# Kernel tuning notes

Hardware: AMD Instinct MI355X
Metric: run time of the kernel (lower is better)

Reference implementation:

```python
import jax, jax.numpy as jnp
import numpy as np

N_NODES = 100000
N_EDGES = 3200000
N_GRAPHS = 512
DIM_H = 128
N_LAYERS = 3
N_CLASSES = 10
BN_EPS = 1e-5


def setup_inputs() -> dict:
    key = jax.random.key(0)
    ks = jax.random.split(key, 16)
    s = 1.0 / np.sqrt(DIM_H)
    x = jax.random.normal(ks[0], (N_NODES, DIM_H), dtype=jnp.float32)
    edge_index = jax.random.randint(ks[1], (2, N_EDGES), 0, N_NODES, dtype=jnp.int64)
    batch = jnp.sort(jax.random.randint(ks[2], (N_NODES,), 0, N_GRAPHS, dtype=jnp.int64))
    W1 = jax.random.uniform(ks[3], (N_LAYERS, DIM_H, DIM_H), jnp.float32, -s, s)
    b1 = jax.random.uniform(ks[4], (N_LAYERS, DIM_H), jnp.float32, -s, s)
    gamma = jnp.ones((N_LAYERS, DIM_H), jnp.float32)
    beta = jnp.zeros((N_LAYERS, DIM_H), jnp.float32)
    rmean = 0.1 * jax.random.normal(ks[5], (N_LAYERS, DIM_H), dtype=jnp.float32)
    rvar = jax.random.uniform(ks[6], (N_LAYERS, DIM_H), jnp.float32, 0.5, 1.5)
    W2 = jax.random.uniform(ks[7], (N_LAYERS, DIM_H, DIM_H), jnp.float32, -s, s)
    b2 = jax.random.uniform(ks[8], (N_LAYERS, DIM_H), jnp.float32, -s, s)
    dcat = DIM_H * N_LAYERS
    sf = 1.0 / np.sqrt(dcat)
    Wfin = jax.random.uniform(ks[9], (dcat, dcat), jnp.float32, -sf, sf)
    bfin = jax.random.uniform(ks[10], (dcat,), jnp.float32, -sf, sf)
    Wout = jax.random.uniform(ks[11], (dcat, N_CLASSES), jnp.float32, -sf, sf)
    bout = jax.random.uniform(ks[12], (N_CLASSES,), jnp.float32, -sf, sf)
    return {"x": x, "edge_index": edge_index, "batch": batch, "num_layers": N_LAYERS,
            "W1": W1, "b1": b1, "gamma": gamma, "beta": beta, "rmean": rmean, "rvar": rvar,
            "W2": W2, "b2": b2, "Wfin": Wfin, "bfin": bfin, "Wout": Wout, "bout": bout}


def reference(x, edge_index, batch, num_layers, W1, b1, gamma, beta, rmean, rvar, W2, b2, Wfin, bfin, Wout, bout):
    src, dst = edge_index[0], edge_index[1]
    h = x
    pooled = []
    for i in range(num_layers):
        # GINConv (eps=0): MLP(x + sum_{j in N(i)} x_j)
        aggr = jax.ops.segment_sum(h[src], dst, num_segments=N_NODES)
        z = (h + aggr) @ W1[i] + b1[i]
        # BatchNorm1d in eval mode (running stats)
        z = gamma[i] * (z - rmean[i]) * jax.lax.rsqrt(rvar[i] + BN_EPS) + beta[i]
        z = jax.nn.relu(z)
        h = jax.nn.relu(z @ W2[i] + b2[i])
        # global_add_pool: segment-sum over graph ids
        pooled.append(jax.ops.segment_sum(h, batch, num_segments=N_GRAPHS))
    h_fin = jnp.concatenate(pooled, axis=1)  # [G, dim_h*num_layers]
    h_fin = jax.nn.relu(h_fin @ Wfin + bfin)
    # dropout p=0.5 is identity in eval mode
    logits = h_fin @ Wout + bout
    return logits, jax.nn.log_softmax(logits, axis=1)
```

## Files before the change

kernel.cpp:

```cpp
#include <hip/hip_runtime.h>
#include <stdint.h>

#define N_NODES 100000
#define N_EDGES 3200000
#define N_GRAPHS 512
#define DIM 128
#define M_PAD 100096
#define NGB (M_PAD / 256)
#define NBUCK 391
#define CAP 9216
#define TILE 4096
#define NTILE 782
#define XMM_NB 392

typedef __bf16 bf16x8 __attribute__((ext_vector_type(8)));
typedef float f32x4 __attribute__((ext_vector_type(4)));

__device__ __forceinline__ unsigned short f2bf(float f) {
  unsigned u = __float_as_uint(f);
  u = u + 0x7FFFu + ((u >> 16) & 1u);
  return (unsigned short)(u >> 16);
}
__device__ __forceinline__ float bflo(unsigned v) { return __uint_as_float(v << 16); }
__device__ __forceinline__ float bfhi(unsigned v) { return __uint_as_float(v & 0xFFFF0000u); }
__device__ __forceinline__ unsigned packbf(float a, float b) {
  return (unsigned)f2bf(a) | ((unsigned)f2bf(b) << 16);
}

__global__ void k_zero32(int* __restrict__ p, int n) {
  int i = blockIdx.x * 256 + threadIdx.x;
  if (i < n) p[i] = 0;
}

__global__ __launch_bounds__(256) void k_bucket(const int* __restrict__ ei,
                                                int* __restrict__ cnt,
                                                unsigned* __restrict__ rec) {
  __shared__ int hist[NBUCK];
  __shared__ int curs[NBUCK];
  int t = threadIdx.x;
  int base_e = blockIdx.x * TILE;
  int es[16], ed[16];
#pragma unroll
  for (int k = 0; k < 16; ++k) {
    int e = base_e + k * 256 + t;
    if (e < N_EDGES) { es[k] = ei[e]; ed[k] = ei[N_EDGES + e]; }
    else ed[k] = -1;
  }
  for (int i = t; i < NBUCK; i += 256) hist[i] = 0;
  __syncthreads();
#pragma unroll
  for (int k = 0; k < 16; ++k)
    if (ed[k] >= 0) atomicAdd(&hist[ed[k] >> 8], 1);
  __syncthreads();
  for (int i = t; i < NBUCK; i += 256) {
    int h = hist[i];
    int g = h ? atomicAdd(&cnt[i], h) : 0;
    curs[i] = i * CAP + g;
  }
  __syncthreads();
#pragma unroll
  for (int k = 0; k < 16; ++k) {
    if (ed[k] >= 0) {
      int b = ed[k] >> 8;
      int pos = atomicAdd(&curs[b], 1);
      rec[pos] = ((unsigned)es[k] << 8) | (unsigned)(ed[k] & 255);
    }
  }
}

__global__ __launch_bounds__(512) void k_bscan(const int* __restrict__ cnt,
                                               int* __restrict__ bbase,
                                               int* __restrict__ row_ptr) {
  __shared__ int sc[512];
  int t = threadIdx.x;
  int tot = (t < NBUCK) ? min(cnt[t], CAP) : 0;
  sc[t] = tot; __syncthreads();
  for (int off = 1; off < 512; off <<= 1) {
    int x = (t >= off) ? sc[t - off] : 0;
    __syncthreads();
    sc[t] += x;
    __syncthreads();
  }
  if (t < NBUCK) bbase[t] = sc[t] - tot;
  if (t == NBUCK - 1) {
    bbase[NBUCK] = sc[t];
    row_ptr[N_NODES] = sc[t];
  }
}

__global__ __launch_bounds__(256) void k_build(const unsigned* __restrict__ rec,
                                               const int* __restrict__ cnt,
                                               const int* __restrict__ bbase,
                                               int* __restrict__ row_ptr,
                                               int* __restrict__ col) {
  __shared__ int hist[256];
  __shared__ int sc[256];
  __shared__ int curs[256];
  int b = blockIdx.x, t = threadIdx.x;
  int n = min(cnt[b], CAP);
  const unsigned* p = rec + (size_t)b * CAP;
  hist[t] = 0; __syncthreads();
  for (int i = t; i < n; i += 256) atomicAdd(&hist[p[i] & 255u], 1);
  __syncthreads();
  int v = hist[t];
  sc[t] = v; __syncthreads();
  for (int off = 1; off < 256; off <<= 1) {
    int x = (t >= off) ? sc[t - off] : 0;
    __syncthreads();
    sc[t] += x;
    __syncthreads();
  }
  int excl = bbase[b] + sc[t] - v;
  int node = (b << 8) + t;
  if (node < N_NODES) row_ptr[node] = excl;
  curs[t] = excl;
  __syncthreads();
  for (int i = t; i < n; i += 256) {
    unsigned w = p[i];
    int pos = atomicAdd(&curs[w & 255u], 1);
    col[pos] = (int)(w >> 8);
  }
}

__global__ void k_gptr(const int* __restrict__ batch, int* __restrict__ gptr) {
  int g = blockIdx.x * 64 + threadIdx.x;
  if (g > N_GRAPHS) return;
  int lo = 0, hi = N_NODES;
  while (lo < hi) { int mid = (lo + hi) >> 1; if (batch[mid] < g) lo = mid + 1; else hi = mid; }
  gptr[g] = lo;
}

__global__ __launch_bounds__(256) void k_xmm1(const float* __restrict__ x,
                                              float* __restrict__ pmax,
                                              float* __restrict__ pmin) {
  __shared__ float smx[8][32][4];
  __shared__ float smn[8][32][4];
  int t = threadIdx.x;
  int c4 = t & 31;
  int ro = t >> 5;
  float mx0 = 0.f, mx1 = 0.f, mx2 = 0.f, mx3 = 0.f;
  float mn0 = 0.f, mn1 = 0.f, mn2 = 0.f, mn3 = 0.f;
  for (int row = blockIdx.x * 8 + ro; row < N_NODES; row += XMM_NB * 8) {
    float4 v = ((const float4*)x)[(size_t)row * 32 + c4];
    mx0 = fmaxf(mx0, v.x); mn0 = fmaxf(mn0, -v.x);
    mx1 = fmaxf(mx1, v.y); mn1 = fmaxf(mn1, -v.y);
    mx2 = fmaxf(mx2, v.z); mn2 = fmaxf(mn2, -v.z);
    mx3 = fmaxf(mx3, v.w); mn3 = fmaxf(mn3, -v.w);
  }
  smx[ro][c4][0] = mx0; smx[ro][c4][1] = mx1; smx[ro][c4][2] = mx2; smx[ro][c4][3] = mx3;
  smn[ro][c4][0] = mn0; smn[ro][c4][1] = mn1; smn[ro][c4][2] = mn2; smn[ro][c4][3] = mn3;
  __syncthreads();
  for (int off = 4; off > 0; off >>= 1) {
    if (ro < off) {
#pragma unroll
      for (int k = 0; k < 4; ++k) {
        smx[ro][c4][k] = fmaxf(smx[ro][c4][k], smx[ro + off][c4][k]);
        smn[ro][c4][k] = fmaxf(smn[ro][c4][k], smn[ro + off][c4][k]);
      }
    }
    __syncthreads();
  }
  if (ro == 0) {
#pragma unroll
    for (int k = 0; k < 4; ++k) {
      pmax[blockIdx.x * 128 + c4 * 4 + k] = smx[0][c4][k];
      pmin[blockIdx.x * 128 + c4 * 4 + k] = smn[0][c4][k];
    }
  }
}

__global__ __launch_bounds__(64) void k_xmm2(const float* __restrict__ pmax,
                                             const float* __restrict__ pmin,
                                             float* __restrict__ xmx,
                                             float* __restrict__ xminf) {
  int c = blockIdx.x & 127;
  int isMin = blockIdx.x >> 7;
  const float* src = isMin ? pmin : pmax;
  int l = threadIdx.x;
  float m = 0.f;
  for (int p2 = l; p2 < XMM_NB; p2 += 64) m = fmaxf(m, src[p2 * 128 + c]);
#pragma unroll
  for (int off = 32; off > 0; off >>= 1) m = fmaxf(m, __shfl_down(m, off));
  if (l == 0) {
    if (isMin) xminf[c] = -m;
    else xmx[c] = m;
  }
}

__global__ __launch_bounds__(64) void k_hred(const float* __restrict__ pmaxb,
                                             float* __restrict__ hmax) {
  int c = blockIdx.x;
  float m = 0.f;
  for (int b = threadIdx.x; b < NGB; b += 64) m = fmaxf(m, pmaxb[(size_t)b * 128 + c]);
#pragma unroll
  for (int off = 32; off > 0; off >>= 1) m = fmaxf(m, __shfl_down(m, off));
  if (threadIdx.x == 0) hmax[c] = m;
}

__global__ void k_convx(const float* __restrict__ x, const float* __restrict__ qmin,
                        const float* __restrict__ qmax, unsigned short* __restrict__ xq) {
  int i = blockIdx.x * 256 + threadIdx.x;
  if (i >= M_PAD * 64) return;
  int lane = i & 63;
  unsigned short o = 0;
  if ((i >> 6) < N_NODES) {
    float mn0 = qmin[2 * lane], mn1 = qmin[2 * lane + 1];
    float r0 = qmax[2 * lane] - mn0, r1 = qmax[2 * lane + 1] - mn1;
    float is0 = r0 > 1e-20f ? 255.f / r0 : 0.f;
    float is1 = r1 > 1e-20f ? 255.f / r1 : 0.f;
    float2 f = ((const float2*)x)[i];
    int q0 = (int)rintf((f.x - mn0) * is0); q0 = min(max(q0, 0), 255);
    int q1 = (int)rintf((f.y - mn1) * is1); q1 = min(max(q1, 0), 255);
    o = (unsigned short)(q0 | (q1 << 8));
  }
  xq[i] = o;
}

__global__ void k_quant(const unsigned* __restrict__ hbf, const float* __restrict__ qmax,
                        unsigned short* __restrict__ hq) {
  int i = blockIdx.x * 256 + threadIdx.x;
  if (i >= M_PAD * 64) return;
  int lane = i & 63;
  float mx0 = qmax[2 * lane], mx1 = qmax[2 * lane + 1];
  float is0 = mx0 > 1e-20f ? 255.f / mx0 : 0.f;
  float is1 = mx1 > 1e-20f ? 255.f / mx1 : 0.f;
  unsigned v = hbf[i];
  int q0 = (int)rintf(bflo(v) * is0); q0 = min(max(q0, 0), 255);
  int q1 = (int)rintf(bfhi(v) * is1); q1 = min(max(q1, 0), 255);
  hq[i] = (unsigned short)(q0 | (q1 << 8));
}

__global__ void k_convw(const float* __restrict__ W1, const float* __restrict__ W2,
                        unsigned short* __restrict__ Wt1, unsigned short* __restrict__ Wt2) {
  int i = blockIdx.x * 256 + threadIdx.x;
  if (i >= 3 * DIM * DIM) return;
  int l = i >> 14, rem = i & 16383, k = rem >> 7, n = rem & 127;
  int o = (l << 14) + (n << 7) + k;
  Wt1[o] = f2bf(W1[i]);
  Wt2[o] = f2bf(W2[i]);
}

__global__ void k_coef(const float* __restrict__ b1, const float* __restrict__ gamma,
                       const float* __restrict__ beta, const float* __restrict__ rmean,
                       const float* __restrict__ rvar, const float* __restrict__ b2,
                       float* __restrict__ sA1, float* __restrict__ sB1,
                       float* __restrict__ sA2, float* __restrict__ sB2) {
  int i = blockIdx.x * 128 + threadIdx.x;
  if (i >= 3 * DIM) return;
  float sa = gamma[i] * rsqrtf(rvar[i] + 1e-5f);
  sA1[i] = sa;
  sB1[i] = fmaf(sa, b1[i] - rmean[i], beta[i]);
  sA2[i] = 1.0f;
  sB2[i] = b2[i];
}

__global__ __launch_bounds__(256) void k_aggr(const unsigned short* __restrict__ hq,
                                              const int* __restrict__ row_ptr,
                                              const int* __restrict__ col,
                                              const float* __restrict__ qmin,
                                              const float* __restrict__ qmax,
                                              unsigned* __restrict__ tmp) {
  const unsigned* hq32 = (const unsigned*)hq;
  int wv = (blockIdx.x << 2) + (threadIdx.x >> 6);
  int lane = threadIdx.x & 63;
  int dw = lane & 31;
  bool hi = lane >= 32;
  if (wv >= M_PAD) return;
  if (wv >= N_NODES) {
    ((uint2*)(tmp + (size_t)wv * 64))[dw] = make_uint2(0u, 0u);
    return;
  }
  unsigned ae = 0u, ao = 0u;
  int s = __builtin_amdgcn_readfirstlane(row_ptr[wv]);
  int e = __builtin_amdgcn_readfirstlane(row_ptr[wv + 1]);
  for (int base = s; base < e; base += 64) {
    int n = e - base; if (n > 64) n = 64;
    int cv = (lane < n) ? col[base + lane] : 0;
    int np = n >> 1;
    int j = 0;
    for (; j + 4 <= np; j += 4) {
#pragma unroll
      for (int u = 0; u < 4; ++u) {
        int s0 = __builtin_amdgcn_readlane(cv, 2 * (j + u));
        int s1 = __builtin_amdgcn_readlane(cv, 2 * (j + u) + 1);
        int a0 = s0 * 32 + dw;
        int a1 = s1 * 32 + dw;
        unsigned v = hq32[hi ? a1 : a0];
        ae += v & 0x00FF00FFu;
        ao += (v >> 8) & 0x00FF00FFu;
      }
    }
    for (; j < np; ++j) {
      int s0 = __builtin_amdgcn_readlane(cv, 2 * j);
      int s1 = __builtin_amdgcn_readlane(cv, 2 * j + 1);
      int a0 = s0 * 32 + dw;
      int a1 = s1 * 32 + dw;
      unsigned v = hq32[hi ? a1 : a0];
      ae += v & 0x00FF00FFu;
      ao += (v >> 8) & 0x00FF00FFu;
    }
    if (n & 1) {
      int c = __builtin_amdgcn_readlane(cv, n - 1);
      unsigned v = hq32[c * 32 + dw];
      if (hi) v = 0u;
      ae += v & 0x00FF00FFu;
      ao += (v >> 8) & 0x00FF00FFu;
    }
  }
  ae += __shfl_xor(ae, 32);
  ao += __shfl_xor(ao, 32);
  {
    unsigned v = hq32[wv * 32 + dw];
    ae += v & 0x00FF00FFu;
    ao += (v >> 8) & 0x00FF00FFu;
  }
  if (lane < 32) {
    float cnt = (float)(e - s + 1);
    float4 qn = ((const float4*)qmin)[dw];
    float4 qx = ((const float4*)qmax)[dw];
    float s0f = (float)(ae & 0xFFFFu);
    float s1f = (float)(ao & 0xFFFFu);
    float s2f = (float)(ae >> 16);
    float s3f = (float)(ao >> 16);
    const float k255 = 1.0f / 255.0f;
    float A0 = fmaf(qn.x, cnt, (qx.x - qn.x) * k255 * s0f);
    float A1 = fmaf(qn.y, cnt, (qx.y - qn.y) * k255 * s1f);
    float A2 = fmaf(qn.z, cnt, (qx.z - qn.z) * k255 * s2f);
    float A3 = fmaf(qn.w, cnt, (qx.w - qn.w) * k255 * s3f);
    ((uint2*)(tmp + (size_t)wv * 64))[dw] = make_uint2(packbf(A0, A1), packbf(A2, A3));
  }
}

__global__ __launch_bounds__(256, 2) void k_gemm12(const unsigned short* __restrict__ A,
                                                   const unsigned short* __restrict__ Wt1,
                                                   const float* __restrict__ sA1,
                                                   const float* __restrict__ sB1,
                                                   const unsigned short* __restrict__ Wt2,
                                                   const float* __restrict__ sA2,
                                                   const float* __restrict__ sB2,
                                                   unsigned short* __restrict__ out,
                                                   float* __restrict__ pmaxb, int do_max) {
  __shared__ unsigned short zt[4][64][136];
  __shared__ float colred[128];
  int w = threadIdx.x >> 6, lane = threadIdx.x & 63;
  int q = lane >> 4, n16 = lane & 15;
  int rbase = (blockIdx.x << 8) + (w << 6);
  if (do_max && threadIdx.x < 128) colred[threadIdx.x] = 0.f;

  {
    bf16x8 Bf[4][8];
#pragma unroll
    for (int ks = 0; ks < 4; ++ks)
#pragma unroll
      for (int c = 0; c < 8; ++c)
        Bf[ks][c] = *(const bf16x8*)(Wt1 + (size_t)((c << 4) + n16) * DIM + ks * 32 + q * 8);
#pragma unroll
    for (int t = 0; t < 4; ++t) {
      int r0 = rbase + (t << 4);
      f32x4 acc[8] = {};
#pragma unroll
      for (int ks = 0; ks < 4; ++ks) {
        bf16x8 a = *(const bf16x8*)(A + (size_t)(r0 + n16) * DIM + ks * 32 + q * 8);
#pragma unroll
        for (int c = 0; c < 8; ++c)
          acc[c] = __builtin_amdgcn_mfma_f32_16x16x32_bf16(a, Bf[ks][c], acc[c], 0, 0, 0);
      }
#pragma unroll
      for (int c = 0; c < 8; ++c) {
        int colc = (c << 4) + n16;
        float s = sA1[colc], tt = sB1[colc];
#pragma unroll
        for (int r = 0; r < 4; ++r) {
          float v = fmaxf(fmaf(s, acc[c][r], tt), 0.0f);
          zt[w][(t << 4) + (q << 2) + r][colc] = f2bf(v);
        }
      }
    }
  }

  {
    bf16x8 Bf[4][8];
#pragma unroll
    for (int ks = 0; ks < 4; ++ks)
#pragma unroll
      for (int c = 0; c < 8; ++c)
        Bf[ks][c] = *(const bf16x8*)(Wt2 + (size_t)((c << 4) + n16) * DIM + ks * 32 + q * 8);
    float mcol[8];
#pragma unroll
    for (int c = 0; c < 8; ++c) mcol[c] = 0.f;
#pragma unroll
    for (int t = 0; t < 4; ++t) {
      int r0 = rbase + (t << 4);
      f32x4 acc[8] = {};
#pragma unroll
      for (int ks = 0; ks < 4; ++ks) {
        bf16x8 a = *(const bf16x8*)(&zt[w][(t << 4) + n16][ks * 32 + q * 8]);
#pragma unroll
        for (int c = 0; c < 8; ++c)
          acc[c] = __builtin_amdgcn_mfma_f32_16x16x32_bf16(a, Bf[ks][c], acc[c], 0, 0, 0);
      }
#pragma unroll
      for (int c = 0; c < 8; ++c) {
        int colc = (c << 4) + n16;
        float s = sA2[colc], tt = sB2[colc];
#pragma unroll
        for (int r = 0; r < 4; ++r) {
          float v = fmaxf(fmaf(s, acc[c][r], tt), 0.0f);
          mcol[c] = fmaxf(mcol[c], v);
          out[(size_t)(r0 + (q << 2) + r) * DIM + colc] = f2bf(v);
        }
      }
    }
    if (do_max) {
      __syncthreads();
#pragma unroll
      for (int c = 0; c < 8; ++c)
        atomicMax((int*)&colred[(c << 4) + n16], __float_as_int(mcol[c]));
      __syncthreads();
      if (threadIdx.x < 128)
        pmaxb[(size_t)blockIdx.x * 128 + threadIdx.x] = colred[threadIdx.x];
    }
  }
}

__global__ __launch_bounds__(256) void k_pool(const unsigned* __restrict__ hbf,
                                              const int* __restrict__ gptr,
                                              float* __restrict__ pooled, int layer) {
  __shared__ float red[4][128];
  int g = blockIdx.x;
  int uc = threadIdx.x & 63, rs = threadIdx.x >> 6;
  int beg = gptr[g], end = gptr[g + 1];
  float a0 = 0.f, a1 = 0.f;
  for (int r = beg + rs; r < end; r += 4) {
    unsigned v = hbf[(size_t)r * 64 + uc];
    a0 += bflo(v); a1 += bfhi(v);
  }
  red[rs][2 * uc] = a0; red[rs][2 * uc + 1] = a1;
  __syncthreads();
  if (rs == 0) {
    int c0 = 2 * uc, c1 = 2 * uc + 1;
    pooled[(size_t)g * 384 + layer * DIM + c0] = red[0][c0] + red[1][c0] + red[2][c0] + red[3][c0];
    pooled[(size_t)g * 384 + layer * DIM + c1] = red[0][c1] + red[1][c1] + red[2][c1] + red[3][c1];
  }
}

__global__ __launch_bounds__(384) void k_head(const float* __restrict__ pooled,
                                              const float* __restrict__ Wfin,
                                              const float* __restrict__ bfin,
                                              const float* __restrict__ Wout,
                                              const float* __restrict__ bout,
                                              float* __restrict__ out) {
  __shared__ float p[8][384];
  __shared__ float hf[8][392];
  __shared__ float lg[8][10];
  __shared__ float lse[8];
  int t = threadIdx.x, g0 = blockIdx.x << 3;
  for (int i = t; i < 8 * 384; i += 384)
    p[i / 384][i % 384] = pooled[(size_t)(g0 + i / 384) * 384 + (i % 384)];
  __syncthreads();
  float bb = bfin[t];
  float acc[8];
#pragma unroll
  for (int g = 0; g < 8; ++g) acc[g] = bb;
  for (int k = 0; k < 384; ++k) {
    float wv = Wfin[k * 384 + t];
#pragma unroll
    for (int g = 0; g < 8; ++g) acc[g] = fmaf(p[g][k], wv, acc[g]);
  }
#pragma unroll
  for (int g = 0; g < 8; ++g) hf[g][t] = fmaxf(acc[g], 0.f);
  __syncthreads();
  if (t < 80) {
    int g = t / 10, c = t % 10;
    float a = bout[c];
    for (int k = 0; k < 384; ++k) a = fmaf(hf[g][k], Wout[k * 10 + c], a);
    lg[g][c] = a;
  }
  __syncthreads();
  if (t < 8) {
    float m = lg[t][0];
#pragma unroll
    for (int i = 1; i < 10; ++i) m = fmaxf(m, lg[t][i]);
    float ss = 0.f;
#pragma unroll
    for (int i = 0; i < 10; ++i) ss += __expf(lg[t][i] - m);
    lse[t] = m + __logf(ss);
  }
  __syncthreads();
  if (t < 80) {
    int g = t / 10, c = t % 10;
    out[(size_t)(g0 + g) * 10 + c] = lg[g][c];
    out[(size_t)N_GRAPHS * 10 + (size_t)(g0 + g) * 10 + c] = lg[g][c] - lse[g];
  }
}

extern "C" void kernel_launch(void* const* d_in, const int* in_sizes, int n_in,
                              void* d_out, int out_size, void* d_ws, size_t ws_size,
                              hipStream_t stream) {
  const float* x     = (const float*)d_in[0];
  const int*   ei    = (const int*)d_in[1];
  const int*   batch = (const int*)d_in[2];
  const float* W1    = (const float*)d_in[4];
  const float* b1    = (const float*)d_in[5];
  const float* gamma = (const float*)d_in[6];
  const float* beta  = (const float*)d_in[7];
  const float* rmean = (const float*)d_in[8];
  const float* rvar  = (const float*)d_in[9];
  const float* W2    = (const float*)d_in[10];
  const float* b2    = (const float*)d_in[11];
  const float* Wfin  = (const float*)d_in[12];
  const float* bfin  = (const float*)d_in[13];
  const float* Wout  = (const float*)d_in[14];
  const float* bout  = (const float*)d_in[15];
  float* out = (float*)d_out;

  char* p = (char*)d_ws;
  auto alloc = [&](size_t bytes) { char* r = p; p += (bytes + 255) & ~255ull; return r; };
  int* cnt      = (int*)alloc(NBUCK * 4);
  unsigned* rec = (unsigned*)alloc((size_t)NBUCK * CAP * 4);
  int* bbase    = (int*)alloc((NBUCK + 1) * 4);
  int* row_ptr  = (int*)alloc((N_NODES + 1) * 4);
  int* colb     = (int*)alloc((size_t)N_EDGES * 4);
  int* gptr     = (int*)alloc((N_GRAPHS + 1) * 4);
  unsigned short* xq  = (unsigned short*)alloc((size_t)M_PAD * 64 * 2);
  unsigned short* hqb = (unsigned short*)alloc((size_t)M_PAD * 64 * 2);
  unsigned* hbf  = (unsigned*)alloc((size_t)M_PAD * 64 * 4);
  unsigned* tmpb = (unsigned*)alloc((size_t)M_PAD * 64 * 4);
  unsigned short* Wt1 = (unsigned short*)alloc(3 * DIM * DIM * 2);
  unsigned short* Wt2 = (unsigned short*)alloc(3 * DIM * DIM * 2);
  float* pmax   = (float*)alloc((size_t)XMM_NB * 128 * 4);
  float* pmin   = (float*)alloc((size_t)XMM_NB * 128 * 4);
  float* pmaxb  = (float*)alloc((size_t)NGB * 128 * 4);
  float* sA1    = (float*)alloc(384 * 4);
  float* sB1    = (float*)alloc(384 * 4);
  float* sA2    = (float*)alloc(384 * 4);
  float* sB2    = (float*)alloc(384 * 4);
  float* qbuf   = (float*)alloc(1024 * 4);
  float* xmx    = qbuf + 128;
  float* xminf  = qbuf + 256;
  float* hmax0  = qbuf + 384;
  float* hmax1  = qbuf + 512;
  float* zeros  = qbuf + 640;
  float* pooled = (float*)alloc((size_t)N_GRAPHS * 384 * 4);

  k_zero32<<<(NBUCK + 255) / 256, 256, 0, stream>>>(cnt, NBUCK);
  k_zero32<<<4, 256, 0, stream>>>((int*)qbuf, 1024);

  k_bucket<<<NTILE, 256, 0, stream>>>(ei, cnt, rec);
  k_bscan<<<1, 512, 0, stream>>>(cnt, bbase, row_ptr);
  k_build<<<NBUCK, 256, 0, stream>>>(rec, cnt, bbase, row_ptr, colb);
  k_gptr<<<9, 64, 0, stream>>>(batch, gptr);

  k_xmm1<<<XMM_NB, 256, 0, stream>>>(x, pmax, pmin);
  k_xmm2<<<256, 64, 0, stream>>>(pmax, pmin, xmx, xminf);
  k_convx<<<(M_PAD * 64 + 255) / 256, 256, 0, stream>>>(x, xminf, xmx, xq);
  k_convw<<<(3 * DIM * DIM + 255) / 256, 256, 0, stream>>>(W1, W2, Wt1, Wt2);
  k_coef<<<3, 128, 0, stream>>>(b1, gamma, beta, rmean, rvar, b2, sA1, sB1, sA2, sB2);

  k_aggr<<<M_PAD / 4, 256, 0, stream>>>(xq, row_ptr, colb, xminf, xmx, tmpb);
  k_gemm12<<<NGB, 256, 0, stream>>>((const unsigned short*)tmpb, Wt1, sA1, sB1,
                                    Wt2, sA2, sB2, (unsigned short*)hbf, pmaxb, 1);
  k_hred<<<128, 64, 0, stream>>>(pmaxb, hmax0);
  k_pool<<<N_GRAPHS, 256, 0, stream>>>(hbf, gptr, pooled, 0);
  k_quant<<<(M_PAD * 64 + 255) / 256, 256, 0, stream>>>(hbf, hmax0, hqb);
  k_aggr<<<M_PAD / 4, 256, 0, stream>>>(hqb, row_ptr, colb, zeros, hmax0, tmpb);
  k_gemm12<<<NGB, 256, 0, stream>>>((const unsigned short*)tmpb, Wt1 + DIM * DIM,
                                    sA1 + DIM, sB1 + DIM, Wt2 + DIM * DIM,
                                    sA2 + DIM, sB2 + DIM, (unsigned short*)hbf, pmaxb, 1);
  k_hred<<<128, 64, 0, stream>>>(pmaxb, hmax1);
  k_pool<<<N_GRAPHS, 256, 0, stream>>>(hbf, gptr, pooled, 1);
  k_quant<<<(M_PAD * 64 + 255) / 256, 256, 0, stream>>>(hbf, hmax1, hqb);
  k_aggr<<<M_PAD / 4, 256, 0, stream>>>(hqb, row_ptr, colb, zeros, hmax1, tmpb);
  k_gemm12<<<NGB, 256, 0, stream>>>((const unsigned short*)tmpb, Wt1 + 2 * DIM * DIM,
                                    sA1 + 2 * DIM, sB1 + 2 * DIM, Wt2 + 2 * DIM * DIM,
                                    sA2 + 2 * DIM, sB2 + 2 * DIM, (unsigned short*)hbf, pmaxb, 0);
  k_pool<<<N_GRAPHS, 256, 0, stream>>>(hbf, gptr, pooled, 2);

  k_head<<<N_GRAPHS / 8, 384, 0, stream>>>(pooled, Wfin, bfin, Wout, bout, out);
}
```

Before: 662.8 us.

## Fuse global add pooling into GEMM epilogue with partitioned atomic accumulators

Removes the separate k_pool and k_gptr kernels. Instead, each GEMM block stages its output tile in shared memory and does a run-length segmented sum over sorted batch ids, atomically adding into one of 8 partitioned pooled copies. The head kernel then sums those copies. The aggregation inner loop is also unrolled from 4 to 8. The change trades extra atomics, a new 6 MB zeroing pass, an s_waitcnt(0) and a serial 128-row loop for fewer launches and no re-read of the hidden activations.

```diff
diff --git a/kernel.cpp b/kernel.cpp
--- a/kernel.cpp
+++ b/kernel.cpp
@@ -23,6 +23,7 @@
 }
 __device__ __forceinline__ float bflo(unsigned v) { return __uint_as_float(v << 16); }
 __device__ __forceinline__ float bfhi(unsigned v) { return __uint_as_float(v & 0xFFFF0000u); }
+__device__ __forceinline__ float bfs(unsigned short v) { return __uint_as_float(((unsigned)v) << 16); }
 __device__ __forceinline__ unsigned packbf(float a, float b) {
   return (unsigned)f2bf(a) | ((unsigned)f2bf(b) << 16);
 }
@@ -120,14 +121,6 @@
     int pos = atomicAdd(&curs[w & 255u], 1);
     col[pos] = (int)(w >> 8);
   }
-}
-
-__global__ void k_gptr(const int* __restrict__ batch, int* __restrict__ gptr) {
-  int g = blockIdx.x * 64 + threadIdx.x;
-  if (g > N_GRAPHS) return;
-  int lo = 0, hi = N_NODES;
-  while (lo < hi) { int mid = (lo + hi) >> 1; if (batch[mid] < g) lo = mid + 1; else hi = mid; }
-  gptr[g] = lo;
 }
 
 __global__ __launch_bounds__(256) void k_xmm1(const float* __restrict__ x,
@@ -278,14 +271,12 @@
     int cv = (lane < n) ? col[base + lane] : 0;
     int np = n >> 1;
     int j = 0;
-    for (; j + 4 <= np; j += 4) {
-#pragma unroll
-      for (int u = 0; u < 4; ++u) {
+    for (; j + 8 <= np; j += 8) {
+#pragma unroll
+      for (int u = 0; u < 8; ++u) {
         int s0 = __builtin_amdgcn_readlane(cv, 2 * (j + u));
         int s1 = __builtin_amdgcn_readlane(cv, 2 * (j + u) + 1);
-        int a0 = s0 * 32 + dw;
-        int a1 = s1 * 32 + dw;
-        unsigned v = hq32[hi ? a1 : a0];
+        unsigned v = hq32[(hi ? s1 : s0) * 32 + dw];
         ae += v & 0x00FF00FFu;
         ao += (v >> 8) & 0x00FF00FFu;
       }
@@ -293,9 +284,7 @@
     for (; j < np; ++j) {
       int s0 = __builtin_amdgcn_readlane(cv, 2 * j);
       int s1 = __builtin_amdgcn_readlane(cv, 2 * j + 1);
-      int a0 = s0 * 32 + dw;
-      int a1 = s1 * 32 + dw;
-      unsigned v = hq32[hi ? a1 : a0];
+      unsigned v = hq32[(hi ? s1 : s0) * 32 + dw];
       ae += v & 0x00FF00FFu;
       ao += (v >> 8) & 0x00FF00FFu;
     }
@@ -318,15 +307,11 @@
     float cnt = (float)(e - s + 1);
     float4 qn = ((const float4*)qmin)[dw];
     float4 qx = ((const float4*)qmax)[dw];
-    float s0f = (float)(ae & 0xFFFFu);
-    float s1f = (float)(ao & 0xFFFFu);
-    float s2f = (float)(ae >> 16);
-    float s3f = (float)(ao >> 16);
     const float k255 = 1.0f / 255.0f;
-    float A0 = fmaf(qn.x, cnt, (qx.x - qn.x) * k255 * s0f);
-    float A1 = fmaf(qn.y, cnt, (qx.y - qn.y) * k255 * s1f);
-    float A2 = fmaf(qn.z, cnt, (qx.z - qn.z) * k255 * s2f);
-    float A3 = fmaf(qn.w, cnt, (qx.w - qn.w) * k255 * s3f);
+    float A0 = fmaf(qn.x, cnt, (qx.x - qn.x) * k255 * (float)(ae & 0xFFFFu));
+    float A1 = fmaf(qn.y, cnt, (qx.y - qn.y) * k255 * (float)(ao & 0xFFFFu));
+    float A2 = fmaf(qn.z, cnt, (qx.z - qn.z) * k255 * (float)(ae >> 16));
+    float A3 = fmaf(qn.w, cnt, (qx.w - qn.w) * k255 * (float)(ao >> 16));
     ((uint2*)(tmp + (size_t)wv * 64))[dw] = make_uint2(packbf(A0, A1), packbf(A2, A3));
   }
 }
@@ -338,14 +323,21 @@
                                                    const unsigned short* __restrict__ Wt2,
                                                    const float* __restrict__ sA2,
                                                    const float* __restrict__ sB2,
+                                                   const int* __restrict__ batch,
                                                    unsigned short* __restrict__ out,
+                                                   float* __restrict__ pooled8, int layer,
                                                    float* __restrict__ pmaxb, int do_max) {
   __shared__ unsigned short zt[4][64][136];
   __shared__ float colred[128];
+  __shared__ int sgid[256];
   int w = threadIdx.x >> 6, lane = threadIdx.x & 63;
   int q = lane >> 4, n16 = lane & 15;
   int rbase = (blockIdx.x << 8) + (w << 6);
   if (do_max && threadIdx.x < 128) colred[threadIdx.x] = 0.f;
+  {
+    int rr = (blockIdx.x << 8) + threadIdx.x;
+    sgid[threadIdx.x] = (rr < N_NODES) ? batch[rr] : -1;
+  }
 
   {
     bf16x8 Bf[4][8];
@@ -378,6 +370,9 @@
     }
   }
 
+  float mcol[8];
+#pragma unroll
+  for (int c = 0; c < 8; ++c) mcol[c] = 0.f;
   {
     bf16x8 Bf[4][8];
 #pragma unroll
@@ -385,9 +380,6 @@
 #pragma unroll
       for (int c = 0; c < 8; ++c)
         Bf[ks][c] = *(const bf16x8*)(Wt2 + (size_t)((c << 4) + n16) * DIM + ks * 32 + q * 8);
-    float mcol[8];
-#pragma unroll
-    for (int c = 0; c < 8; ++c) mcol[c] = 0.f;
 #pragma unroll
     for (int t = 0; t < 4; ++t) {
       int r0 = rbase + (t << 4);
@@ -399,6 +391,7 @@
         for (int c = 0; c < 8; ++c)
           acc[c] = __builtin_amdgcn_mfma_f32_16x16x32_bf16(a, Bf[ks][c], acc[c], 0, 0, 0);
       }
+      __builtin_amdgcn_s_waitcnt(0);
 #pragma unroll
       for (int c = 0; c < 8; ++c) {
         int colc = (c << 4) + n16;
@@ -407,44 +400,46 @@
         for (int r = 0; r < 4; ++r) {
           float v = fmaxf(fmaf(s, acc[c][r], tt), 0.0f);
           mcol[c] = fmaxf(mcol[c], v);
-          out[(size_t)(r0 + (q << 2) + r) * DIM + colc] = f2bf(v);
+          unsigned short hv = f2bf(v);
+          out[(size_t)(r0 + (q << 2) + r) * DIM + colc] = hv;
+          zt[w][(t << 4) + (q << 2) + r][colc] = hv;
         }
       }
     }
-    if (do_max) {
-      __syncthreads();
-#pragma unroll
-      for (int c = 0; c < 8; ++c)
-        atomicMax((int*)&colred[(c << 4) + n16], __float_as_int(mcol[c]));
-      __syncthreads();
-      if (threadIdx.x < 128)
-        pmaxb[(size_t)blockIdx.x * 128 + threadIdx.x] = colred[threadIdx.x];
-    }
-  }
-}
-
-__global__ __launch_bounds__(256) void k_pool(const unsigned* __restrict__ hbf,
-                                              const int* __restrict__ gptr,
-                                              float* __restrict__ pooled, int layer) {
-  __shared__ float red[4][128];
-  int g = blockIdx.x;
-  int uc = threadIdx.x & 63, rs = threadIdx.x >> 6;
-  int beg = gptr[g], end = gptr[g + 1];
-  float a0 = 0.f, a1 = 0.f;
-  for (int r = beg + rs; r < end; r += 4) {
-    unsigned v = hbf[(size_t)r * 64 + uc];
-    a0 += bflo(v); a1 += bfhi(v);
-  }
-  red[rs][2 * uc] = a0; red[rs][2 * uc + 1] = a1;
-  __syncthreads();
-  if (rs == 0) {
-    int c0 = 2 * uc, c1 = 2 * uc + 1;
-    pooled[(size_t)g * 384 + layer * DIM + c0] = red[0][c0] + red[1][c0] + red[2][c0] + red[3][c0];
-    pooled[(size_t)g * 384 + layer * DIM + c1] = red[0][c1] + red[1][c1] + red[2][c1] + red[3][c1];
-  }
-}
-
-__global__ __launch_bounds__(384) void k_head(const float* __restrict__ pooled,
+  }
+  __syncthreads();
+
+  {
+    const unsigned short* ztf = &zt[0][0][0];
+    int colp = threadIdx.x & 127, grp = threadIdx.x >> 7;
+    int cp = blockIdx.x & 7;
+    float pacc = 0.f;
+    int gcur = sgid[grp << 7];
+    for (int r = 0; r < 128; ++r) {
+      int row = (grp << 7) + r;
+      int g = sgid[row];
+      if (g != gcur) {
+        if (gcur >= 0)
+          atomicAdd(&pooled8[((size_t)cp * N_GRAPHS + gcur) * 384 + layer * DIM + colp], pacc);
+        pacc = 0.f; gcur = g;
+      }
+      if (g >= 0) pacc += bfs(ztf[row * 136 + colp]);
+    }
+    if (gcur >= 0)
+      atomicAdd(&pooled8[((size_t)cp * N_GRAPHS + gcur) * 384 + layer * DIM + colp], pacc);
+  }
+
+  if (do_max) {
+#pragma unroll
+    for (int c = 0; c < 8; ++c)
+      atomicMax((int*)&colred[(c << 4) + n16], __float_as_int(mcol[c]));
+    __syncthreads();
+    if (threadIdx.x < 128)
+      pmaxb[(size_t)blockIdx.x * 128 + threadIdx.x] = colred[threadIdx.x];
+  }
+}
+
+__global__ __launch_bounds__(384) void k_head(const float* __restrict__ pooled8,
                                               const float* __restrict__ Wfin,
                                               const float* __restrict__ bfin,
                                               const float* __restrict__ Wout,
@@ -455,8 +450,14 @@
   __shared__ float lg[8][10];
   __shared__ float lse[8];
   int t = threadIdx.x, g0 = blockIdx.x << 3;
-  for (int i = t; i < 8 * 384; i += 384)
-    p[i / 384][i % 384] = pooled[(size_t)(g0 + i / 384) * 384 + (i % 384)];
+  for (int i = t; i < 8 * 384; i += 384) {
+    int gl = i / 384, k = i % 384;
+    float s = 0.f;
+#pragma unroll
+    for (int cp = 0; cp < 8; ++cp)
+      s += pooled8[((size_t)cp * N_GRAPHS + g0 + gl) * 384 + k];
+    p[gl][k] = s;
+  }
   __syncthreads();
   float bb = bfin[t];
   float acc[8];
@@ -521,7 +522,6 @@
   int* bbase    = (int*)alloc((NBUCK + 1) * 4);
   int* row_ptr  = (int*)alloc((N_NODES + 1) * 4);
   int* colb     = (int*)alloc((size_t)N_EDGES * 4);
-  int* gptr     = (int*)alloc((N_GRAPHS + 1) * 4);
   unsigned short* xq  = (unsigned short*)alloc((size_t)M_PAD * 64 * 2);
   unsigned short* hqb = (unsigned short*)alloc((size_t)M_PAD * 64 * 2);
   unsigned* hbf  = (unsigned*)alloc((size_t)M_PAD * 64 * 4);
@@ -541,15 +541,15 @@
   float* hmax0  = qbuf + 384;
   float* hmax1  = qbuf + 512;
   float* zeros  = qbuf + 640;
-  float* pooled = (float*)alloc((size_t)N_GRAPHS * 384 * 4);
+  float* pooled8 = (float*)alloc((size_t)8 * N_GRAPHS * 384 * 4);
 
   k_zero32<<<(NBUCK + 255) / 256, 256, 0, stream>>>(cnt, NBUCK);
   k_zero32<<<4, 256, 0, stream>>>((int*)qbuf, 1024);
+  k_zero32<<<(8 * N_GRAPHS * 384 + 255) / 256, 256, 0, stream>>>((int*)pooled8, 8 * N_GRAPHS * 384);
 
   k_bucket<<<NTILE, 256, 0, stream>>>(ei, cnt, rec);
   k_bscan<<<1, 512, 0, stream>>>(cnt, bbase, row_ptr);
   k_build<<<NBUCK, 256, 0, stream>>>(rec, cnt, bbase, row_ptr, colb);
-  k_gptr<<<9, 64, 0, stream>>>(batch, gptr);
 
   k_xmm1<<<XMM_NB, 256, 0, stream>>>(x, pmax, pmin);
   k_xmm2<<<256, 64, 0, stream>>>(pmax, pmin, xmx, xminf);
@@ -559,22 +559,22 @@
 
   k_aggr<<<M_PAD / 4, 256, 0, stream>>>(xq, row_ptr, colb, xminf, xmx, tmpb);
   k_gemm12<<<NGB, 256, 0, stream>>>((const unsigned short*)tmpb, Wt1, sA1, sB1,
-                                    Wt2, sA2, sB2, (unsigned short*)hbf, pmaxb, 1);
+                                    Wt2, sA2, sB2, batch, (unsigned short*)hbf,
+                                    pooled8, 0, pmaxb, 1);
   k_hred<<<128, 64, 0, stream>>>(pmaxb, hmax0);
-  k_pool<<<N_GRAPHS, 256, 0, stream>>>(hbf, gptr, pooled, 0);
   k_quant<<<(M_PAD * 64 + 255) / 256, 256, 0, stream>>>(hbf, hmax0, hqb);
   k_aggr<<<M_PAD / 4, 256, 0, stream>>>(hqb, row_ptr, colb, zeros, hmax0, tmpb);
   k_gemm12<<<NGB, 256, 0, stream>>>((const unsigned short*)tmpb, Wt1 + DIM * DIM,
                                     sA1 + DIM, sB1 + DIM, Wt2 + DIM * DIM,
-                                    sA2 + DIM, sB2 + DIM, (unsigned short*)hbf, pmaxb, 1);
+                                    sA2 + DIM, sB2 + DIM, batch, (unsigned short*)hbf,
+                                    pooled8, 1, pmaxb, 1);
   k_hred<<<128, 64, 0, stream>>>(pmaxb, hmax1);
-  k_pool<<<N_GRAPHS, 256, 0, stream>>>(hbf, gptr, pooled, 1);
   k_quant<<<(M_PAD * 64 + 255) / 256, 256, 0, stream>>>(hbf, hmax1, hqb);
   k_aggr<<<M_PAD / 4, 256, 0, stream>>>(hqb, row_ptr, colb, zeros, hmax1, tmpb);
   k_gemm12<<<NGB, 256, 0, stream>>>((const unsigned short*)tmpb, Wt1 + 2 * DIM * DIM,
                                     sA1 + 2 * DIM, sB1 + 2 * DIM, Wt2 + 2 * DIM * DIM,
-                                    sA2 + 2 * DIM, sB2 + 2 * DIM, (unsigned short*)hbf, pmaxb, 0);
-  k_pool<<<N_GRAPHS, 256, 0, stream>>>(hbf, gptr, pooled, 2);
-
-  k_head<<<N_GRAPHS / 8, 384, 0, stream>>>(pooled, Wfin, bfin, Wout, bout, out);
-}
+                                    sA2 + 2 * DIM, sB2 + 2 * DIM, batch, (unsigned short*)hbf,
+                                    pooled8, 2, pmaxb, 0);
+
+  k_head<<<N_GRAPHS / 8, 384, 0, stream>>>(pooled8, Wfin, bfin, Wout, bout, out);
+}
```

After: 657.3 us. About the same (-0.8%).
